# Optimization experiments

Hardware: AMD Instinct MI355X
Metric: run time of the kernel (lower is better)

## Reference

```python
import jax, jax.numpy as jnp
import numpy as np

DIMS = [64, 32, 12, 8, 6, 2]


def setup_inputs() -> dict:
    key = jax.random.key(0)
    ks = jax.random.split(key, 1 + 2 * (len(DIMS) - 1))
    inp = {"x": jax.random.normal(ks[0], (1048576, DIMS[0]), dtype=jnp.float32)}
    for i in range(len(DIMS) - 1):
        fan_in = DIMS[i]
        bound = 1.0 / np.sqrt(fan_in)
        inp[f"W{i}"] = jax.random.uniform(ks[1 + 2 * i], (DIMS[i], DIMS[i + 1]), jnp.float32, -bound, bound)
        inp[f"b{i}"] = jax.random.uniform(ks[2 + 2 * i], (DIMS[i + 1],), jnp.float32, -bound, bound)
    return inp


def reference(x, W0, b0, W1, b1, W2, b2, W3, b3, W4, b4):
    # 5-layer Linear+ReLU chain (final layer has no ReLU), matching nn.Sequential.
    h = jax.nn.relu(x @ W0 + b0)
    h = jax.nn.relu(h @ W1 + b1)
    h = jax.nn.relu(h @ W2 + b2)
    h = jax.nn.relu(h @ W3 + b3)
    return h @ W4 + b4  # [B, 2]
```

## Files before the change

kernel.cpp:

```cpp
#include <hip/hip_runtime.h>


typedef __attribute__((ext_vector_type(8))) short short8;
typedef __attribute__((ext_vector_type(16))) float f32x16;
typedef __attribute__((ext_vector_type(4))) unsigned uint4v;
typedef __attribute__((address_space(3))) void* as3p;
typedef const __attribute__((address_space(1))) void* as1p;

#define BLOCK 64
#define NT 4

__device__ __forceinline__ unsigned fbits(float x) {
    return __builtin_bit_cast(unsigned, x);
}
__device__ __forceinline__ float asf(unsigned u) {
    return __builtin_bit_cast(float, u);
}
__device__ __forceinline__ unsigned packhi(unsigned ua, unsigned ub) {
    return __builtin_amdgcn_perm(ub, ua, 0x07060302u);
}
__device__ __forceinline__ short8 mk_hi(const float* f) {
    uint4v w;
#pragma unroll
    for (int t = 0; t < 4; ++t)
        w[t] = packhi(fbits(f[2 * t]), fbits(f[2 * t + 1]));
    return __builtin_bit_cast(short8, w);
}
__device__ __forceinline__ short8 mk_lo(const float* f) {
    uint4v w;
#pragma unroll
    for (int t = 0; t < 4; ++t) {
        const float la = f[2 * t]     - asf(fbits(f[2 * t])     & 0xFFFF0000u);
        const float lb = f[2 * t + 1] - asf(fbits(f[2 * t + 1]) & 0xFFFF0000u);
        w[t] = packhi(fbits(la), fbits(lb));
    }
    return __builtin_bit_cast(short8, w);
}
#define MFMA(A, B, C) __builtin_amdgcn_mfma_f32_32x32x16_bf16(A, B, C, 0, 0, 0)

template <int IN, int OUT, bool RELU>
__device__ __forceinline__ void layer(const float* __restrict__ W,
                                      const float* __restrict__ b,
                                      const float* h_in, float* h_out) {
#pragma unroll
    for (int o = 0; o < OUT; ++o) h_out[o] = b[o];
#pragma unroll
    for (int i = 0; i < IN; ++i) {
        const float v = h_in[i];
#pragma unroll
        for (int o = 0; o < OUT; ++o)
            h_out[o] = fmaf(v, W[i * OUT + o], h_out[o]);
    }
    if (RELU) {
#pragma unroll
        for (int o = 0; o < OUT; ++o) h_out[o] = fmaxf(h_out[o], 0.0f);
    }
}

__global__ __launch_bounds__(BLOCK, 2) void mlp_kernel(
        const float* __restrict__ x,
        const float* __restrict__ W0, const float* __restrict__ b0,
        const float* __restrict__ W1, const float* __restrict__ b1,
        const float* __restrict__ W2, const float* __restrict__ b2,
        const float* __restrict__ W3, const float* __restrict__ b3,
        const float* __restrict__ W4, const float* __restrict__ b4,
        float* __restrict__ out, int nrows) {
    extern __shared__ char lds[];
    char* buf0 = lds;
    char* buf1 = lds + 4096;
    char* h0b  = lds + 8192;

    const int lane = threadIdx.x;
    const long long row0 = (long long)blockIdx.x * (NT * 64);
    const char* xbase = reinterpret_cast<const char*>(x + row0 * 64);

    const int hh = lane >> 3;
    const int qq = (lane & 7) ^ hh;
    const int stage_off = (2 * hh + (qq >> 2)) * 256 + (qq & 3) * 16;

    const int r0 = lane & 31;
    const int hA = lane >> 5;
    auto lds_off = [](int r, int u) {
        const int R = r >> 1, p = r & 1;
        return R * 128 + (((u + 4 * p) ^ (R & 7)) << 4);
    };
    const int aoff0 = lds_off(r0, 2 * hA);
    const int aoff1 = lds_off(r0, 2 * hA + 1);
    const int aoff2 = lds_off(r0 + 32, 2 * hA);
    const int aoff3 = lds_off(r0 + 32, 2 * hA + 1);

    const int colB = lane & 31;
    short8 B0h, B0l, B1h, B1l, B2h, B2l, B3h, B3l;
    {
        float wf[8];
#define LOADB(c, BH, BL)                                                \
        {                                                               \
            _Pragma("unroll")                                           \
            for (int j = 0; j < 8; ++j)                                 \
                wf[j] = W0[((c) * 16 + 8 * hA + j) * 32 + colB];        \
            BH = mk_hi(wf);                                             \
            BL = mk_lo(wf);                                             \
        }
        LOADB(0, B0h, B0l)
        LOADB(1, B1h, B1l)
        LOADB(2, B2h, B2l)
        LOADB(3, B3h, B3l)
#undef LOADB
    }
    const float vb0 = b0[colB];

    auto STAGE = [&](int gc, char* buf) {
        const char* s0 = xbase + (gc >> 2) * (64 * 256) + (gc & 3) * 64 +
                         stage_off;
#pragma unroll
        for (int k = 0; k < 4; ++k)
            __builtin_amdgcn_global_load_lds((as1p)(s0 + k * 4096),
                                             (as3p)(buf + k * 1024), 16, 0, 0);
    };

    STAGE(0, buf0);

#pragma unroll 1
    for (int tt = 0; tt < NT; ++tt) {
        f32x16 accA, accB;
#pragma unroll
        for (int r = 0; r < 16; ++r) { accA[r] = vb0; accB[r] = vb0; }

#define CHUNK_BODY(CUR, BH, BL)                                            \
        {                                                                  \
            float fA[8], fB[8];                                            \
            const float4 q0 = *reinterpret_cast<const float4*>(CUR + aoff0); \
            const float4 q1 = *reinterpret_cast<const float4*>(CUR + aoff1); \
            const float4 q2 = *reinterpret_cast<const float4*>(CUR + aoff2); \
            const float4 q3 = *reinterpret_cast<const float4*>(CUR + aoff3); \
            fA[0]=q0.x; fA[1]=q0.y; fA[2]=q0.z; fA[3]=q0.w;                \
            fA[4]=q1.x; fA[5]=q1.y; fA[6]=q1.z; fA[7]=q1.w;                \
            fB[0]=q2.x; fB[1]=q2.y; fB[2]=q2.z; fB[3]=q2.w;                \
            fB[4]=q3.x; fB[5]=q3.y; fB[6]=q3.z; fB[7]=q3.w;                \
            const short8 Ah = mk_hi(fA), Al = mk_lo(fA);                   \
            const short8 Ch = mk_hi(fB), Cl = mk_lo(fB);                   \
            accA = MFMA(Ah, BH, accA);                                     \
            accA = MFMA(Al, BH, accA);                                     \
            accA = MFMA(Ah, BL, accA);                                     \
            accB = MFMA(Ch, BH, accB);                                     \
            accB = MFMA(Cl, BH, accB);                                     \
            accB = MFMA(Ch, BL, accB);                                     \
        }
#define PHASE(c, BH, BL)                                                   \
        {                                                                  \
            const int gc = tt * 4 + (c);                                   \
            char* cur = ((c) & 1) ? buf1 : buf0;                           \
            char* oth = ((c) & 1) ? buf0 : buf1;                           \
            if (gc + 1 < NT * 4) {                                         \
                STAGE(gc + 1, oth);                                        \
                asm volatile("s_waitcnt vmcnt(4)" ::: "memory");           \
            } else {                                                       \
                asm volatile("s_waitcnt vmcnt(0)" ::: "memory");           \
            }                                                              \
            __builtin_amdgcn_sched_barrier(0);                             \
            CHUNK_BODY(cur, BH, BL)                                        \
        }

        PHASE(0, B0h, B0l)
        PHASE(1, B1h, B1l)
        PHASE(2, B2h, B2l)
        PHASE(3, B3h, B3l)
#undef PHASE
#undef CHUNK_BODY

#pragma unroll
        for (int reg = 0; reg < 16; ++reg) {
            const int r1 = (reg & 3) + 8 * (reg >> 2) + 4 * hA;
            const int r2 = r1 + 32;
            const int w1 = r1 * 128 + (((colB >> 2) ^ (r1 & 7)) << 4) +
                           (colB & 3) * 4;
            const int w2 = r2 * 128 + (((colB >> 2) ^ (r2 & 7)) << 4) +
                           (colB & 3) * 4;
            *reinterpret_cast<float*>(h0b + w1) = fmaxf(accA[reg], 0.0f);
            *reinterpret_cast<float*>(h0b + w2) = fmaxf(accB[reg], 0.0f);
        }

        float xr[32];
#pragma unroll
        for (int u = 0; u < 8; ++u) {
            const int slot = u ^ (lane & 7);
            const float4 q = *reinterpret_cast<const float4*>(
                h0b + lane * 128 + slot * 16);
            xr[4 * u + 0] = q.x; xr[4 * u + 1] = q.y;
            xr[4 * u + 2] = q.z; xr[4 * u + 3] = q.w;
        }

        float h1[12], h2[8], h3[6], h4[2];
        layer<32, 12, true>(W1, b1, xr, h1);
        layer<12, 8, true>(W2, b2, h1, h2);
        layer<8, 6, true>(W3, b3, h2, h3);
        layer<6, 2, false>(W4, b4, h3, h4);

        reinterpret_cast<float2*>(out)[row0 + tt * 64 + lane] =
            make_float2(h4[0], h4[1]);
    }
}

extern "C" void kernel_launch(void* const* d_in, const int* in_sizes, int n_in,
                              void* d_out, int out_size, void* d_ws, size_t ws_size,
                              hipStream_t stream) {
    const float* x  = (const float*)d_in[0];
    const float* W0 = (const float*)d_in[1];
    const float* b0 = (const float*)d_in[2];
    const float* W1 = (const float*)d_in[3];
    const float* b1 = (const float*)d_in[4];
    const float* W2 = (const float*)d_in[5];
    const float* b2 = (const float*)d_in[6];
    const float* W3 = (const float*)d_in[7];
    const float* b3 = (const float*)d_in[8];
    const float* W4 = (const float*)d_in[9];
    const float* b4 = (const float*)d_in[10];
    float* out = (float*)d_out;

    const int nrows = in_sizes[0] / 64;
    const int rows_per_block = NT * 64;
    const int grid = nrows / rows_per_block;
    const size_t shmem = 16384;

    mlp_kernel<<<grid, BLOCK, shmem, stream>>>(x, W0, b0, W1, b1, W2, b2,
                                               W3, b3, W4, b4, out, nrows);
}
```

Measured before the change: 64.93 us.

## Use two waves per block and reuse staging buffer for layer-0 output

Each block now runs two independent wavefronts, each handling its own row range and its own 8KB LDS slice. The separate 4KB h0 buffer is removed: the layer-0 activations are written into the second staging buffer in two 32-row halves, with each half-wave reading its rows between writes. This cuts LDS per wave so more waves can be resident (launch bounds raised to 4). The cost is an extra lgkmcnt wait and a serialized two-step write/read of the activations. Reusing buf1 also assumes the last staging load into that buffer has completed before it is overwritten.

```diff
diff --git a/kernel.cpp b/kernel.cpp
--- a/kernel.cpp
+++ b/kernel.cpp
@@ -7,7 +7,7 @@
 typedef __attribute__((address_space(3))) void* as3p;
 typedef const __attribute__((address_space(1))) void* as1p;
 
-#define BLOCK 64
+#define BLOCK 128
 #define NT 4
 
 __device__ __forceinline__ unsigned fbits(float x) {
@@ -57,7 +57,7 @@
     }
 }
 
-__global__ __launch_bounds__(BLOCK, 2) void mlp_kernel(
+__global__ __launch_bounds__(BLOCK, 4) void mlp_kernel(
         const float* __restrict__ x,
         const float* __restrict__ W0, const float* __restrict__ b0,
         const float* __restrict__ W1, const float* __restrict__ b1,
@@ -66,12 +66,13 @@
         const float* __restrict__ W4, const float* __restrict__ b4,
         float* __restrict__ out, int nrows) {
     extern __shared__ char lds[];
-    char* buf0 = lds;
-    char* buf1 = lds + 4096;
-    char* h0b  = lds + 8192;
-
-    const int lane = threadIdx.x;
-    const long long row0 = (long long)blockIdx.x * (NT * 64);
+    const int t = threadIdx.x;
+    const int wv = t >> 6;
+    const int lane = t & 63;
+    char* buf0 = lds + wv * 8192;
+    char* buf1 = buf0 + 4096;
+
+    const long long row0 = ((long long)blockIdx.x * 2 + wv) * (NT * 64);
     const char* xbase = reinterpret_cast<const char*>(x + row0 * 64);
 
     const int hh = lane >> 3;
@@ -168,26 +169,45 @@
 #undef PHASE
 #undef CHUNK_BODY
 
+        float xr[32];
+
 #pragma unroll
         for (int reg = 0; reg < 16; ++reg) {
             const int r1 = (reg & 3) + 8 * (reg >> 2) + 4 * hA;
-            const int r2 = r1 + 32;
             const int w1 = r1 * 128 + (((colB >> 2) ^ (r1 & 7)) << 4) +
                            (colB & 3) * 4;
+            *reinterpret_cast<float*>(buf1 + w1) = fmaxf(accA[reg], 0.0f);
+        }
+        if (lane < 32) {
+#pragma unroll
+            for (int u = 0; u < 8; ++u) {
+                const int slot = u ^ (lane & 7);
+                const float4 qv = *reinterpret_cast<const float4*>(
+                    buf1 + lane * 128 + slot * 16);
+                xr[4 * u + 0] = qv.x; xr[4 * u + 1] = qv.y;
+                xr[4 * u + 2] = qv.z; xr[4 * u + 3] = qv.w;
+            }
+        }
+        asm volatile("s_waitcnt lgkmcnt(0)" ::: "memory");
+        __builtin_amdgcn_sched_barrier(0);
+
+#pragma unroll
+        for (int reg = 0; reg < 16; ++reg) {
+            const int r2 = (reg & 3) + 8 * (reg >> 2) + 4 * hA;
             const int w2 = r2 * 128 + (((colB >> 2) ^ (r2 & 7)) << 4) +
                            (colB & 3) * 4;
-            *reinterpret_cast<float*>(h0b + w1) = fmaxf(accA[reg], 0.0f);
-            *reinterpret_cast<float*>(h0b + w2) = fmaxf(accB[reg], 0.0f);
-        }
-
-        float xr[32];
-#pragma unroll
-        for (int u = 0; u < 8; ++u) {
-            const int slot = u ^ (lane & 7);
-            const float4 q = *reinterpret_cast<const float4*>(
-                h0b + lane * 128 + slot * 16);
-            xr[4 * u + 0] = q.x; xr[4 * u + 1] = q.y;
-            xr[4 * u + 2] = q.z; xr[4 * u + 3] = q.w;
+            *reinterpret_cast<float*>(buf1 + w2) = fmaxf(accB[reg], 0.0f);
+        }
+        if (lane >= 32) {
+            const int r = lane & 31;
+#pragma unroll
+            for (int u = 0; u < 8; ++u) {
+                const int slot = u ^ (r & 7);
+                const float4 qv = *reinterpret_cast<const float4*>(
+                    buf1 + r * 128 + slot * 16);
+                xr[4 * u + 0] = qv.x; xr[4 * u + 1] = qv.y;
+                xr[4 * u + 2] = qv.z; xr[4 * u + 3] = qv.w;
+            }
         }
 
         float h1[12], h2[8], h3[6], h4[2];
@@ -218,9 +238,9 @@
     float* out = (float*)d_out;
 
     const int nrows = in_sizes[0] / 64;
-    const int rows_per_block = NT * 64;
+    const int rows_per_block = 2 * NT * 64;
     const int grid = nrows / rows_per_block;
-    const size_t shmem = 16384;
+    const size_t shmem = 2 * 8192;
 
     mlp_kernel<<<grid, BLOCK, shmem, stream>>>(x, W0, b0, W1, b1, W2, b2,
                                                W3, b3, W4, b4, out, nrows);
```

Measured after the change: 138.3 us. 2.13x slower.

## Transpose MFMA operands and redistribute layer-0 output with permlane32 swap instead of LDS

Applied to the files above, without the earlier changes.

Swaps the A/B operand roles in the first-layer MFMAs so the accumulator holds rows along lanes, then uses v_permlane32_swap to give each lane its own row's 32 features directly. This removes the LDS round-trip (store, then swizzled reload) for the hidden activation, halves the dynamic shared memory, and raises the launch-bounds occupancy hint from 2 to 4. The bias is now added after the swap using per-feature scalar loads, and the tighter occupancy hint may constrain register allocation.

```diff
diff --git a/kernel.cpp b/kernel.cpp
--- a/kernel.cpp
+++ b/kernel.cpp
@@ -57,7 +57,7 @@
     }
 }
 
-__global__ __launch_bounds__(BLOCK, 2) void mlp_kernel(
+__global__ __launch_bounds__(BLOCK, 4) void mlp_kernel(
         const float* __restrict__ x,
         const float* __restrict__ W0, const float* __restrict__ b0,
         const float* __restrict__ W1, const float* __restrict__ b1,
@@ -68,7 +68,6 @@
     extern __shared__ char lds[];
     char* buf0 = lds;
     char* buf1 = lds + 4096;
-    char* h0b  = lds + 8192;
 
     const int lane = threadIdx.x;
     const long long row0 = (long long)blockIdx.x * (NT * 64);
@@ -90,7 +89,7 @@
     const int aoff3 = lds_off(r0 + 32, 2 * hA + 1);
 
     const int colB = lane & 31;
-    short8 B0h, B0l, B1h, B1l, B2h, B2l, B3h, B3l;
+    short8 W0h_, W0l_, W1h_, W1l_, W2h_, W2l_, W3h_, W3l_;
     {
         float wf[8];
 #define LOADB(c, BH, BL)                                                \
@@ -101,13 +100,12 @@
             BH = mk_hi(wf);                                             \
             BL = mk_lo(wf);                                             \
         }
-        LOADB(0, B0h, B0l)
-        LOADB(1, B1h, B1l)
-        LOADB(2, B2h, B2l)
-        LOADB(3, B3h, B3l)
+        LOADB(0, W0h_, W0l_)
+        LOADB(1, W1h_, W1l_)
+        LOADB(2, W2h_, W2l_)
+        LOADB(3, W3h_, W3l_)
 #undef LOADB
     }
-    const float vb0 = b0[colB];
 
     auto STAGE = [&](int gc, char* buf) {
         const char* s0 = xbase + (gc >> 2) * (64 * 256) + (gc & 3) * 64 +
@@ -124,9 +122,9 @@
     for (int tt = 0; tt < NT; ++tt) {
         f32x16 accA, accB;
 #pragma unroll
-        for (int r = 0; r < 16; ++r) { accA[r] = vb0; accB[r] = vb0; }
-
-#define CHUNK_BODY(CUR, BH, BL)                                            \
+        for (int r = 0; r < 16; ++r) { accA[r] = 0.0f; accB[r] = 0.0f; }
+
+#define CHUNK_BODY(CUR, WH, WL)                                            \
         {                                                                  \
             float fA[8], fB[8];                                            \
             const float4 q0 = *reinterpret_cast<const float4*>(CUR + aoff0); \
@@ -137,16 +135,16 @@
             fA[4]=q1.x; fA[5]=q1.y; fA[6]=q1.z; fA[7]=q1.w;                \
             fB[0]=q2.x; fB[1]=q2.y; fB[2]=q2.z; fB[3]=q2.w;                \
             fB[4]=q3.x; fB[5]=q3.y; fB[6]=q3.z; fB[7]=q3.w;                \
-            const short8 Ah = mk_hi(fA), Al = mk_lo(fA);                   \
-            const short8 Ch = mk_hi(fB), Cl = mk_lo(fB);                   \
-            accA = MFMA(Ah, BH, accA);                                     \
-            accA = MFMA(Al, BH, accA);                                     \
-            accA = MFMA(Ah, BL, accA);                                     \
-            accB = MFMA(Ch, BH, accB);                                     \
-            accB = MFMA(Cl, BH, accB);                                     \
-            accB = MFMA(Ch, BL, accB);                                     \
-        }
-#define PHASE(c, BH, BL)                                                   \
+            const short8 Xh = mk_hi(fA), Xl = mk_lo(fA);                   \
+            const short8 Yh = mk_hi(fB), Yl = mk_lo(fB);                   \
+            accA = MFMA(WH, Xh, accA);                                     \
+            accA = MFMA(WL, Xh, accA);                                     \
+            accA = MFMA(WH, Xl, accA);                                     \
+            accB = MFMA(WH, Yh, accB);                                     \
+            accB = MFMA(WL, Yh, accB);                                     \
+            accB = MFMA(WH, Yl, accB);                                     \
+        }
+#define PHASE(c, WH, WL)                                                   \
         {                                                                  \
             const int gc = tt * 4 + (c);                                   \
             char* cur = ((c) & 1) ? buf1 : buf0;                           \
@@ -158,36 +156,25 @@
                 asm volatile("s_waitcnt vmcnt(0)" ::: "memory");           \
             }                                                              \
             __builtin_amdgcn_sched_barrier(0);                             \
-            CHUNK_BODY(cur, BH, BL)                                        \
-        }
-
-        PHASE(0, B0h, B0l)
-        PHASE(1, B1h, B1l)
-        PHASE(2, B2h, B2l)
-        PHASE(3, B3h, B3l)
+            CHUNK_BODY(cur, WH, WL)                                        \
+        }
+
+        PHASE(0, W0h_, W0l_)
+        PHASE(1, W1h_, W1l_)
+        PHASE(2, W2h_, W2l_)
+        PHASE(3, W3h_, W3l_)
 #undef PHASE
 #undef CHUNK_BODY
 
+        float xr[32];
 #pragma unroll
         for (int reg = 0; reg < 16; ++reg) {
-            const int r1 = (reg & 3) + 8 * (reg >> 2) + 4 * hA;
-            const int r2 = r1 + 32;
-            const int w1 = r1 * 128 + (((colB >> 2) ^ (r1 & 7)) << 4) +
-                           (colB & 3) * 4;
-            const int w2 = r2 * 128 + (((colB >> 2) ^ (r2 & 7)) << 4) +
-                           (colB & 3) * 4;
-            *reinterpret_cast<float*>(h0b + w1) = fmaxf(accA[reg], 0.0f);
-            *reinterpret_cast<float*>(h0b + w2) = fmaxf(accB[reg], 0.0f);
-        }
-
-        float xr[32];
-#pragma unroll
-        for (int u = 0; u < 8; ++u) {
-            const int slot = u ^ (lane & 7);
-            const float4 q = *reinterpret_cast<const float4*>(
-                h0b + lane * 128 + slot * 16);
-            xr[4 * u + 0] = q.x; xr[4 * u + 1] = q.y;
-            xr[4 * u + 2] = q.z; xr[4 * u + 3] = q.w;
+            float a = accA[reg];
+            float b = accB[reg];
+            asm("v_permlane32_swap_b32 %0, %1" : "+v"(a), "+v"(b));
+            const int f0 = (reg & 3) + 8 * (reg >> 2);
+            xr[f0]     = fmaxf(a + b0[f0],     0.0f);
+            xr[f0 + 4] = fmaxf(b + b0[f0 + 4], 0.0f);
         }
 
         float h1[12], h2[8], h3[6], h4[2];
@@ -220,7 +207,7 @@
     const int nrows = in_sizes[0] / 64;
     const int rows_per_block = NT * 64;
     const int grid = nrows / rows_per_block;
-    const size_t shmem = 16384;
+    const size_t shmem = 8192;
 
     mlp_kernel<<<grid, BLOCK, shmem, stream>>>(x, W0, b0, W1, b1, W2, b2,
                                                W3, b3, W4, b4, out, nrows);
```

Measured after the change: 66.86 us, median of 2. +3.0%, slower.
